# Optimization experiments

Hardware: AMD Instinct MI355X
Metric: run time of the kernel (lower is better)

Reference implementation:

```python
import jax, jax.numpy as jnp
import numpy as np

N_NODES = 50000
N_EDGES = 800000
IN_FEATS = 128
H_FEATS = 128
OUT_FEATS = 64


def _mean_agg(h, src, dst, n_nodes):
    # mean over in-neighbors: sum h[src] into dst, divide by in-degree (0 for isolated nodes)
    summed = jax.ops.segment_sum(h[src], dst, num_segments=n_nodes)  # [N, d]
    deg = jax.ops.segment_sum(jnp.ones((src.shape[0],), h.dtype), dst, num_segments=n_nodes)
    return summed / jnp.maximum(deg, 1.0)[:, None]


def setup_inputs() -> dict:
    key = jax.random.key(0)
    ks = jax.random.split(key, 10)
    s = 0.05
    return {
        "inputs": jax.random.normal(ks[0], (N_NODES, IN_FEATS), jnp.float32),
        "fc_W": jax.random.normal(ks[1], (H_FEATS, IN_FEATS), jnp.float32) * s,
        "fc_b": jax.random.normal(ks[2], (H_FEATS,), jnp.float32) * s,
        "W": jax.random.normal(ks[3], (3, H_FEATS, H_FEATS), jnp.float32) * s,
        "b": jax.random.normal(ks[4], (3, H_FEATS), jnp.float32) * s,
        "W_last": jax.random.normal(ks[5], (OUT_FEATS, H_FEATS), jnp.float32) * s,
        "b_last": jax.random.normal(ks[6], (OUT_FEATS,), jnp.float32) * s,
        "eps": jnp.zeros((4,), jnp.float32),
        "src": jax.random.randint(ks[7], (N_EDGES,), 0, N_NODES, jnp.int32),
        "dst": jax.random.randint(ks[8], (N_EDGES,), 0, N_NODES, jnp.int32),
    }


def reference(inputs, fc_W, fc_b, W, b, W_last, b_last, eps, src, dst):
    n = inputs.shape[0]
    # input SLP
    h = jax.nn.relu(inputs @ fc_W.T + fc_b)
    # 3 hidden GIN layers: relu(Linear((1+eps)*h + mean_agg(h)))  (dropout = eval identity)
    for i in range(3):
        agg = _mean_agg(h, src, dst, n)
        h = jax.nn.relu(((1.0 + eps[i]) * h + agg) @ W[i].T + b[i])
    # last GIN layer (no ReLU)
    agg = _mean_agg(h, src, dst, n)
    h = ((1.0 + eps[3]) * h + agg) @ W_last.T + b_last
    return h
```

## Files before the change

### kernel.cpp

```cpp
#include <hip/hip_runtime.h>

#define N_NODES 50000
#define N_EDGES 800000
#define NBUCK 196
#define CAP 4608
#define CSTRIDE 16
#define EPB 4096
#define NSTRIPE ((N_EDGES + EPB - 1) / EPB)

typedef __attribute__((ext_vector_type(8))) short short8;
typedef __attribute__((ext_vector_type(4))) float float4v;

__device__ inline unsigned short f2bf(float f) {
    unsigned u = __float_as_uint(f);
    unsigned r = u + 0x7fff + ((u >> 16) & 1);
    return (unsigned short)(r >> 16);
}
__device__ inline float bf2f(unsigned short h) {
    return __uint_as_float(((unsigned)h) << 16);
}


__global__ void __launch_bounds__(256) wsplit_init(
    const float* __restrict__ fcW, const float* __restrict__ W, const float* __restrict__ Wl,
    unsigned short* __restrict__ hi, unsigned short* __restrict__ lo, int* __restrict__ cursor) {
    if (blockIdx.x == 0) {
        for (int j = threadIdx.x; j < NBUCK * CSTRIDE; j += 256) cursor[j] = 0;
    }
    int i = blockIdx.x * 256 + threadIdx.x;
    float v;
    if (i < 16384) v = fcW[i];
    else if (i < 65536) v = W[i - 16384];
    else if (i < 73728) v = Wl[i - 65536];
    else return;
    unsigned short h = f2bf(v);
    hi[i] = h;
    lo[i] = f2bf(v - bf2f(h));
}


template <int COLS, bool RELU, bool WRITE_BF, bool BIAS, bool ASPLIT>
__device__ __forceinline__ void gemm_body(int bx, const float* __restrict__ U,
                                          const unsigned short* __restrict__ Uhi,
                                          const unsigned short* __restrict__ Ulo,
                                          const unsigned short* __restrict__ Whi,
                                          const unsigned short* __restrict__ Wlo,
                                          const float* __restrict__ bias, float* __restrict__ out,
                                          unsigned short* __restrict__ outbf, int nrows) {
    int wave = threadIdx.x >> 6;
    int lane = threadIdx.x & 63;
    int m = lane & 15;
    int quad = lane >> 4;
    int r0 = bx * 64 + wave * 16;
    int rowA = r0 + m;
    if (rowA >= nrows) rowA = nrows - 1;

    short8 ahi[4], alo[4];
    if (ASPLIT) {
        const unsigned short* hp = Uhi + (size_t)rowA * 128 + quad * 8;
        const unsigned short* lp = Ulo + (size_t)rowA * 128 + quad * 8;
#pragma unroll
        for (int kc = 0; kc < 4; kc++) {
            ahi[kc] = *(const short8*)(hp + kc * 32);
            alo[kc] = *(const short8*)(lp + kc * 32);
        }
    } else {
        const float* arow = U + (size_t)rowA * 128 + quad * 8;
#pragma unroll
        for (int kc = 0; kc < 4; kc++) {
            float4 f0 = *(const float4*)(arow + kc * 32);
            float4 f1 = *(const float4*)(arow + kc * 32 + 4);
            float fv[8] = {f0.x, f0.y, f0.z, f0.w, f1.x, f1.y, f1.z, f1.w};
#pragma unroll
            for (int j = 0; j < 8; j++) {
                unsigned short h = f2bf(fv[j]);
                ahi[kc][j] = (short)h;
                alo[kc][j] = (short)f2bf(fv[j] - bf2f(h));
            }
        }
    }

#pragma unroll
    for (int nt = 0; nt < COLS / 16; nt++) {
        int n = nt * 16 + m;
        const unsigned short* bhp = Whi + (size_t)n * 128 + quad * 8;
        const unsigned short* blp = Wlo + (size_t)n * 128 + quad * 8;
        float4v acc = {0.f, 0.f, 0.f, 0.f};
#pragma unroll
        for (int kc = 0; kc < 4; kc++) {
            short8 bh = *(const short8*)(bhp + kc * 32);
            short8 bl = *(const short8*)(blp + kc * 32);
            acc = __builtin_amdgcn_mfma_f32_16x16x32_bf16(ahi[kc], bh, acc, 0, 0, 0);
            acc = __builtin_amdgcn_mfma_f32_16x16x32_bf16(alo[kc], bh, acc, 0, 0, 0);
            acc = __builtin_amdgcn_mfma_f32_16x16x32_bf16(ahi[kc], bl, acc, 0, 0, 0);
        }
        float bv = 0.f;
        if (BIAS) bv = bias[n];
#pragma unroll
        for (int i = 0; i < 4; i++) {
            int r = r0 + quad * 4 + i;
            if (r < nrows) {
                float v = acc[i] + bv;
                if (RELU) v = fmaxf(v, 0.f);
                out[(size_t)r * COLS + n] = v;
                if (WRITE_BF) outbf[(size_t)r * COLS + n] = f2bf(v);
            }
        }
    }
}

template <int COLS, bool RELU, bool WRITE_BF, bool BIAS, bool ASPLIT>
__global__ void __launch_bounds__(256) gemm_mfma(const float* __restrict__ U,
                                                 const unsigned short* __restrict__ Uhi,
                                                 const unsigned short* __restrict__ Ulo,
                                                 const unsigned short* __restrict__ Whi,
                                                 const unsigned short* __restrict__ Wlo,
                                                 const float* __restrict__ bias,
                                                 float* __restrict__ out,
                                                 unsigned short* __restrict__ outbf, int nrows) {
    gemm_body<COLS, RELU, WRITE_BF, BIAS, ASPLIT>(blockIdx.x, U, Uhi, Ulo, Whi, Wlo, bias, out,
                                                  outbf, nrows);
}


__global__ void __launch_bounds__(256) fused_binA_gemm(
    const int* __restrict__ src, const int* __restrict__ dst, int* __restrict__ cursor,
    int* __restrict__ packed, const float* __restrict__ X, const unsigned short* __restrict__ whi,
    const unsigned short* __restrict__ wlo, const float* __restrict__ fcb, float* __restrict__ h,
    unsigned short* __restrict__ hbf) {
    int bx = blockIdx.x;
    if (bx < NSTRIPE) {
        __shared__ int lcount[256];
        __shared__ int lbase[256];
        int t = threadIdx.x;
        lcount[t] = 0;
        __syncthreads();
        int base = bx * EPB + t;
#pragma unroll 4
        for (int k = 0; k < EPB / 256; k++) {
            int i = base + k * 256;
            if (i < N_EDGES) atomicAdd(&lcount[((unsigned)dst[i]) >> 8], 1);
        }
        __syncthreads();
        if (t < NBUCK) {
            lbase[t] = t * CAP + atomicAdd(&cursor[t * CSTRIDE], lcount[t]);
            lcount[t] = 0;
        }
        __syncthreads();
#pragma unroll 4
        for (int k = 0; k < EPB / 256; k++) {
            int i = base + k * 256;
            if (i < N_EDGES) {
                int d = dst[i];
                int wb = ((unsigned)d) >> 8;
                int p = lbase[wb] + atomicAdd(&lcount[wb], 1);
                if (p < (wb + 1) * CAP)
                    packed[p] = ((d & 255) << 16) | src[i];
            }
        }
    } else {
        gemm_body<128, true, true, true, false>(bx - NSTRIPE, X, nullptr, nullptr, whi, wlo, fcb,
                                                h, hbf, N_NODES);
    }
}


__global__ void __launch_bounds__(256) binB_kernel(const int* __restrict__ packed,
                                                   const int* __restrict__ cursor,
                                                   int* __restrict__ row_ptr,
                                                   int* __restrict__ esrc) {
    __shared__ int sm[256];
    __shared__ int cntS[256];
    __shared__ int curs[256];
    int b = blockIdx.x;
    int t = threadIdx.x;
    int cnt = (t < NBUCK) ? cursor[t * CSTRIDE] : 0;
    cntS[t] = cnt;
    sm[t] = cnt;
    __syncthreads();
    for (int o = 1; o < 256; o <<= 1) {
        int x = sm[t];
        int a = (t >= o) ? sm[t - o] : 0;
        __syncthreads();
        sm[t] = x + a;
        __syncthreads();
    }
    int w0 = sm[b] - cntS[b];
    int mycnt = cntS[b];
    int total = sm[NBUCK - 1];
    __syncthreads();
    if (b == NBUCK - 1 && t == 0) row_ptr[N_NODES] = total;
    int e0r = b * CAP, e1r = b * CAP + mycnt;
    curs[t] = 0;
    __syncthreads();
    for (int i = e0r + t; i < e1r; i += 256) atomicAdd(&curs[((unsigned)packed[i]) >> 16], 1);
    __syncthreads();
    int v = curs[t];
    sm[t] = v;
    __syncthreads();
    for (int o = 1; o < 256; o <<= 1) {
        int x = sm[t];
        int a = (t >= o) ? sm[t - o] : 0;
        __syncthreads();
        sm[t] = x + a;
        __syncthreads();
    }
    int excl = sm[t] - v;
    curs[t] = excl;
    int node = b * 256 + t;
    if (node < N_NODES) row_ptr[node] = w0 + excl;
    __syncthreads();
    for (int i = e0r + t; i < e1r; i += 256) {
        unsigned w = (unsigned)packed[i];
        int p = atomicAdd(&curs[w >> 16], 1);
        esrc[w0 + p] = (int)(w & 0xFFFFu);
    }
}


__global__ void __launch_bounds__(256) agg_kernel(
    const float* __restrict__ h, const unsigned short* __restrict__ hbf,
    const int* __restrict__ row_ptr, const int* __restrict__ esrc,
    const float* __restrict__ eps, int layer, unsigned* __restrict__ uhi32,
    unsigned* __restrict__ ulo32) {
    int gtid = blockIdx.x * 256 + threadIdx.x;
    int node = gtid >> 6;
    int lane = threadIdx.x & 63;
    if (node >= N_NODES) return;
    node = __builtin_amdgcn_readfirstlane(node);
    int beg = __builtin_amdgcn_readfirstlane(row_ptr[node]);
    int end = __builtin_amdgcn_readfirstlane(row_ptr[node + 1]);
    int eg = lane >> 4;
    int fo = lane & 15;

    float a0[8] = {0.f, 0.f, 0.f, 0.f, 0.f, 0.f, 0.f, 0.f};
    float a1[8] = {0.f, 0.f, 0.f, 0.f, 0.f, 0.f, 0.f, 0.f};
    float a2[8] = {0.f, 0.f, 0.f, 0.f, 0.f, 0.f, 0.f, 0.f};
    float a3[8] = {0.f, 0.f, 0.f, 0.f, 0.f, 0.f, 0.f, 0.f};
    int e = beg;
    for (; e + 15 < end; e += 16) {
        int s0 = esrc[e + eg];
        int s1 = esrc[e + 4 + eg];
        int s2 = esrc[e + 8 + eg];
        int s3 = esrc[e + 12 + eg];
        short8 v0 = *(const short8*)(hbf + (size_t)s0 * 128 + fo * 8);
        short8 v1 = *(const short8*)(hbf + (size_t)s1 * 128 + fo * 8);
        short8 v2 = *(const short8*)(hbf + (size_t)s2 * 128 + fo * 8);
        short8 v3 = *(const short8*)(hbf + (size_t)s3 * 128 + fo * 8);
#pragma unroll
        for (int j = 0; j < 8; j++) a0[j] += bf2f((unsigned short)v0[j]);
#pragma unroll
        for (int j = 0; j < 8; j++) a1[j] += bf2f((unsigned short)v1[j]);
#pragma unroll
        for (int j = 0; j < 8; j++) a2[j] += bf2f((unsigned short)v2[j]);
#pragma unroll
        for (int j = 0; j < 8; j++) a3[j] += bf2f((unsigned short)v3[j]);
    }
    if (e + 7 < end) {
        int s0 = esrc[e + eg];
        int s1 = esrc[e + 4 + eg];
        short8 v0 = *(const short8*)(hbf + (size_t)s0 * 128 + fo * 8);
        short8 v1 = *(const short8*)(hbf + (size_t)s1 * 128 + fo * 8);
#pragma unroll
        for (int j = 0; j < 8; j++) a0[j] += bf2f((unsigned short)v0[j]);
#pragma unroll
        for (int j = 0; j < 8; j++) a1[j] += bf2f((unsigned short)v1[j]);
        e += 8;
    }
    if (e + 3 < end) {
        int s = esrc[e + eg];
        short8 v = *(const short8*)(hbf + (size_t)s * 128 + fo * 8);
#pragma unroll
        for (int j = 0; j < 8; j++) a2[j] += bf2f((unsigned short)v[j]);
        e += 4;
    }
    int rem = end - e;
    if (eg < rem) {
        int s = esrc[e + eg];
        short8 v = *(const short8*)(hbf + (size_t)s * 128 + fo * 8);
#pragma unroll
        for (int j = 0; j < 8; j++) a3[j] += bf2f((unsigned short)v[j]);
    }
#pragma unroll
    for (int j = 0; j < 8; j++) {
        float s = (a0[j] + a1[j]) + (a2[j] + a3[j]);
        s += __shfl_xor(s, 16);
        s += __shfl_xor(s, 32);
        a0[j] = s;
    }
    if (eg == 0) {
        int d = end - beg;
        float inv = (d > 0) ? 1.0f / (float)d : 0.0f;
        float ep = 1.0f + eps[layer];
        const float* hr = h + (size_t)node * 128 + fo * 8;
        float4 h0 = *(const float4*)hr;
        float4 h1 = *(const float4*)(hr + 4);
        float hv[8] = {h0.x, h0.y, h0.z, h0.w, h1.x, h1.y, h1.z, h1.w};
        unsigned hip[4], lop[4];
#pragma unroll
        for (int jj = 0; jj < 4; jj++) {
            float ux = ep * hv[2 * jj] + a0[2 * jj] * inv;
            float uy = ep * hv[2 * jj + 1] + a0[2 * jj + 1] * inv;
            unsigned short uh0 = f2bf(ux), uh1 = f2bf(uy);
            hip[jj] = (unsigned)uh0 | ((unsigned)uh1 << 16);
            lop[jj] = (unsigned)f2bf(ux - bf2f(uh0)) | ((unsigned)f2bf(uy - bf2f(uh1)) << 16);
        }
        uint4* ph = (uint4*)(uhi32 + (size_t)node * 64 + fo * 4);
        uint4* pl = (uint4*)(ulo32 + (size_t)node * 64 + fo * 4);
        *ph = make_uint4(hip[0], hip[1], hip[2], hip[3]);
        *pl = make_uint4(lop[0], lop[1], lop[2], lop[3]);
    }
}


__global__ void __launch_bounds__(256) agg64_out(
    const float* __restrict__ g, const unsigned short* __restrict__ gbf,
    const int* __restrict__ row_ptr, const int* __restrict__ esrc,
    const float* __restrict__ eps, const float* __restrict__ bl, float* __restrict__ out) {
    int gtid = blockIdx.x * 256 + threadIdx.x;
    int node = gtid >> 6;
    if (node >= N_NODES) return;
    int lane = threadIdx.x & 63;
    node = __builtin_amdgcn_readfirstlane(node);
    int beg = __builtin_amdgcn_readfirstlane(row_ptr[node]);
    int end = __builtin_amdgcn_readfirstlane(row_ptr[node + 1]);
    int eg = lane >> 3;
    int fo = lane & 7;

    float a0[8] = {0.f, 0.f, 0.f, 0.f, 0.f, 0.f, 0.f, 0.f};
    float a1[8] = {0.f, 0.f, 0.f, 0.f, 0.f, 0.f, 0.f, 0.f};
    float a2[8] = {0.f, 0.f, 0.f, 0.f, 0.f, 0.f, 0.f, 0.f};
    float a3[8] = {0.f, 0.f, 0.f, 0.f, 0.f, 0.f, 0.f, 0.f};
    int e = beg;
    for (; e + 31 < end; e += 32) {
        int s0 = esrc[e + eg];
        int s1 = esrc[e + 8 + eg];
        int s2 = esrc[e + 16 + eg];
        int s3 = esrc[e + 24 + eg];
        short8 v0 = *(const short8*)(gbf + (size_t)s0 * 64 + fo * 8);
        short8 v1 = *(const short8*)(gbf + (size_t)s1 * 64 + fo * 8);
        short8 v2 = *(const short8*)(gbf + (size_t)s2 * 64 + fo * 8);
        short8 v3 = *(const short8*)(gbf + (size_t)s3 * 64 + fo * 8);
#pragma unroll
        for (int j = 0; j < 8; j++) a0[j] += bf2f((unsigned short)v0[j]);
#pragma unroll
        for (int j = 0; j < 8; j++) a1[j] += bf2f((unsigned short)v1[j]);
#pragma unroll
        for (int j = 0; j < 8; j++) a2[j] += bf2f((unsigned short)v2[j]);
#pragma unroll
        for (int j = 0; j < 8; j++) a3[j] += bf2f((unsigned short)v3[j]);
    }
    if (e + 15 < end) {
        int s0 = esrc[e + eg];
        int s1 = esrc[e + 8 + eg];
        short8 v0 = *(const short8*)(gbf + (size_t)s0 * 64 + fo * 8);
        short8 v1 = *(const short8*)(gbf + (size_t)s1 * 64 + fo * 8);
#pragma unroll
        for (int j = 0; j < 8; j++) a0[j] += bf2f((unsigned short)v0[j]);
#pragma unroll
        for (int j = 0; j < 8; j++) a1[j] += bf2f((unsigned short)v1[j]);
        e += 16;
    }
    if (e + 7 < end) {
        int s = esrc[e + eg];
        short8 v = *(const short8*)(gbf + (size_t)s * 64 + fo * 8);
#pragma unroll
        for (int j = 0; j < 8; j++) a2[j] += bf2f((unsigned short)v[j]);
        e += 8;
    }
    int rem = end - e;
    if (eg < rem) {
        int s = esrc[e + eg];
        short8 v = *(const short8*)(gbf + (size_t)s * 64 + fo * 8);
#pragma unroll
        for (int j = 0; j < 8; j++) a3[j] += bf2f((unsigned short)v[j]);
    }
#pragma unroll
    for (int j = 0; j < 8; j++) {
        float s = (a0[j] + a1[j]) + (a2[j] + a3[j]);
        s += __shfl_xor(s, 8);
        s += __shfl_xor(s, 16);
        s += __shfl_xor(s, 32);
        a0[j] = s;
    }
    if (eg == 0) {
        int d = end - beg;
        float inv = (d > 0) ? 1.0f / (float)d : 0.0f;
        float ep = 1.0f + eps[3];
        const float* gr = g + (size_t)node * 64 + fo * 8;
        float4 g0 = *(const float4*)gr;
        float4 g1 = *(const float4*)(gr + 4);
        const float* blr = bl + fo * 8;
        float4 b0 = *(const float4*)blr;
        float4 b1 = *(const float4*)(blr + 4);
        float4 r0, r1;
        r0.x = ep * g0.x + a0[0] * inv + b0.x;
        r0.y = ep * g0.y + a0[1] * inv + b0.y;
        r0.z = ep * g0.z + a0[2] * inv + b0.z;
        r0.w = ep * g0.w + a0[3] * inv + b0.w;
        r1.x = ep * g1.x + a0[4] * inv + b1.x;
        r1.y = ep * g1.y + a0[5] * inv + b1.y;
        r1.z = ep * g1.z + a0[6] * inv + b1.z;
        r1.w = ep * g1.w + a0[7] * inv + b1.w;
        float* op = out + (size_t)node * 64 + fo * 8;
        *(float4*)op = r0;
        *(float4*)(op + 4) = r1;
    }
}


extern "C" void kernel_launch(void* const* d_in, const int* in_sizes, int n_in,
                              void* d_out, int out_size, void* d_ws, size_t ws_size,
                              hipStream_t stream) {
    const float* X   = (const float*)d_in[0];
    const float* fcW = (const float*)d_in[1];
    const float* fcb = (const float*)d_in[2];
    const float* W   = (const float*)d_in[3];
    const float* b   = (const float*)d_in[4];
    const float* Wl  = (const float*)d_in[5];
    const float* bl  = (const float*)d_in[6];
    const float* eps = (const float*)d_in[7];
    const int* src   = (const int*)d_in[8];
    const int* dst   = (const int*)d_in[9];
    float* out = (float*)d_out;

    float* h = (float*)d_ws;
    unsigned short* hbf = (unsigned short*)(h + (size_t)N_NODES * 128);
    unsigned short* uhi = hbf + (size_t)N_NODES * 128;
    unsigned short* ulo = uhi + (size_t)N_NODES * 128;
    unsigned short* whi = ulo + (size_t)N_NODES * 128;
    unsigned short* wlo = whi + 73728;
    int* cursor  = (int*)(wlo + 73728);
    int* row_ptr = cursor + NBUCK * CSTRIDE;
    int* packed  = row_ptr + N_NODES + 1;
    int* esrc    = packed + NBUCK * CAP;
    float* g = (float*)uhi;
    unsigned short* gbf = ulo;

    const int gemm_blocks = (N_NODES + 63) / 64;
    const int agg_blocks = (N_NODES * 64 + 255) / 256;
    const int prep_blocks = (73728 + 255) / 256;

    wsplit_init<<<prep_blocks, 256, 0, stream>>>(fcW, W, Wl, whi, wlo, cursor);
    fused_binA_gemm<<<NSTRIPE + gemm_blocks, 256, 0, stream>>>(src, dst, cursor, packed, X, whi,
                                                               wlo, fcb, h, hbf);
    binB_kernel<<<NBUCK, 256, 0, stream>>>(packed, cursor, row_ptr, esrc);

    for (int i = 0; i < 3; i++) {
        agg_kernel<<<agg_blocks, 256, 0, stream>>>(h, hbf, row_ptr, esrc, eps, i,
                                                   (unsigned*)uhi, (unsigned*)ulo);
        if (i < 2)
            gemm_mfma<128, true, true, true, true><<<gemm_blocks, 256, 0, stream>>>(
                nullptr, uhi, ulo, whi + 16384 + (size_t)i * 16384,
                wlo + 16384 + (size_t)i * 16384, b + (size_t)i * 128, h, hbf, N_NODES);
        else
            gemm_mfma<128, true, false, true, true><<<gemm_blocks, 256, 0, stream>>>(
                nullptr, uhi, ulo, whi + 16384 + (size_t)i * 16384,
                wlo + 16384 + (size_t)i * 16384, b + (size_t)i * 128, h, nullptr, N_NODES);
    }

    gemm_mfma<64, false, true, false, false><<<gemm_blocks, 256, 0, stream>>>(
        h, nullptr, nullptr, whi + 65536, wlo + 65536, nullptr, g, gbf, N_NODES);
    agg64_out<<<agg_blocks, 256, 0, stream>>>(g, gbf, row_ptr, esrc, eps, bl, out);
}
```

Measured before the change: 410.4 us.

## Fuse neighbor aggregation with layer GEMM and final projection per node tile

Each hidden layer now runs as one kernel. A block of 512 threads gathers and mean-aggregates 16 nodes, splits the combined input into bf16 hi/lo parts in swizzled LDS, and runs the 128-wide MFMA GEMM straight from LDS. This removes the global round-trip of the split activations and one launch per layer. The last hidden layer also chains the W_last projection from LDS, and the bf16 features ping-pong between two buffers. Weight splitting and cursor zeroing move into the first fused kernel and a memset, so there are fewer launches. In exchange, the GEMM tiles are small and every block re-reads the weights from cache.

Result: faster. 387.6 us (-5.6%).

```diff
diff --git a/kernel.cpp b/kernel.cpp
--- a/kernel.cpp
+++ b/kernel.cpp
@@ -7,6 +7,8 @@
 #define CSTRIDE 16
 #define EPB 4096
 #define NSTRIPE ((N_EDGES + EPB - 1) / EPB)
+#define GEMMB 782
+#define WSPLB 224
 
 typedef __attribute__((ext_vector_type(8))) short short8;
 typedef __attribute__((ext_vector_type(4))) float float4v;
@@ -20,113 +22,128 @@
     return __uint_as_float(((unsigned)h) << 16);
 }
 
-
-__global__ void __launch_bounds__(256) wsplit_init(
-    const float* __restrict__ fcW, const float* __restrict__ W, const float* __restrict__ Wl,
-    unsigned short* __restrict__ hi, unsigned short* __restrict__ lo, int* __restrict__ cursor) {
-    if (blockIdx.x == 0) {
-        for (int j = threadIdx.x; j < NBUCK * CSTRIDE; j += 256) cursor[j] = 0;
-    }
-    int i = blockIdx.x * 256 + threadIdx.x;
-    float v;
-    if (i < 16384) v = fcW[i];
-    else if (i < 65536) v = W[i - 16384];
-    else if (i < 73728) v = Wl[i - 65536];
-    else return;
-    unsigned short h = f2bf(v);
-    hi[i] = h;
-    lo[i] = f2bf(v - bf2f(h));
-}
-
-
-template <int COLS, bool RELU, bool WRITE_BF, bool BIAS, bool ASPLIT>
-__device__ __forceinline__ void gemm_body(int bx, const float* __restrict__ U,
-                                          const unsigned short* __restrict__ Uhi,
-                                          const unsigned short* __restrict__ Ulo,
-                                          const unsigned short* __restrict__ Whi,
-                                          const unsigned short* __restrict__ Wlo,
-                                          const float* __restrict__ bias, float* __restrict__ out,
-                                          unsigned short* __restrict__ outbf, int nrows) {
+__device__ __forceinline__ void split8(const float* __restrict__ p, short8& hi8, short8& lo8) {
+    float4 f0 = *(const float4*)p;
+    float4 f1 = *(const float4*)(p + 4);
+    float fv[8] = {f0.x, f0.y, f0.z, f0.w, f1.x, f1.y, f1.z, f1.w};
+#pragma unroll
+    for (int j = 0; j < 8; j++) {
+        unsigned short hh = f2bf(fv[j]);
+        hi8[j] = (short)hh;
+        lo8[j] = (short)f2bf(fv[j] - bf2f(hh));
+    }
+}
+
+
+__device__ __forceinline__ void gather_sum(const unsigned short* __restrict__ bf,
+                                           const int* __restrict__ esrc, int beg, int end,
+                                           int eg, int fo, float a0[8]) {
+    float a1[8], a2[8], a3[8];
+#pragma unroll
+    for (int j = 0; j < 8; j++) { a0[j] = 0.f; a1[j] = 0.f; a2[j] = 0.f; a3[j] = 0.f; }
+    int e = beg;
+    for (; e + 15 < end; e += 16) {
+        int s0 = esrc[e + eg];
+        int s1 = esrc[e + 4 + eg];
+        int s2 = esrc[e + 8 + eg];
+        int s3 = esrc[e + 12 + eg];
+        short8 v0 = *(const short8*)(bf + (size_t)s0 * 128 + fo * 8);
+        short8 v1 = *(const short8*)(bf + (size_t)s1 * 128 + fo * 8);
+        short8 v2 = *(const short8*)(bf + (size_t)s2 * 128 + fo * 8);
+        short8 v3 = *(const short8*)(bf + (size_t)s3 * 128 + fo * 8);
+#pragma unroll
+        for (int j = 0; j < 8; j++) a0[j] += bf2f((unsigned short)v0[j]);
+#pragma unroll
+        for (int j = 0; j < 8; j++) a1[j] += bf2f((unsigned short)v1[j]);
+#pragma unroll
+        for (int j = 0; j < 8; j++) a2[j] += bf2f((unsigned short)v2[j]);
+#pragma unroll
+        for (int j = 0; j < 8; j++) a3[j] += bf2f((unsigned short)v3[j]);
+    }
+    if (e + 7 < end) {
+        int s0 = esrc[e + eg];
+        int s1 = esrc[e + 4 + eg];
+        short8 v0 = *(const short8*)(bf + (size_t)s0 * 128 + fo * 8);
+        short8 v1 = *(const short8*)(bf + (size_t)s1 * 128 + fo * 8);
+#pragma unroll
+        for (int j = 0; j < 8; j++) a0[j] += bf2f((unsigned short)v0[j]);
+#pragma unroll
+        for (int j = 0; j < 8; j++) a1[j] += bf2f((unsigned short)v1[j]);
+        e += 8;
+    }
+    if (e + 3 < end) {
+        int s = esrc[e + eg];
+        short8 v = *(const short8*)(bf + (size_t)s * 128 + fo * 8);
+#pragma unroll
+        for (int j = 0; j < 8; j++) a2[j] += bf2f((unsigned short)v[j]);
+        e += 4;
+    }
+    int rem = end - e;
+    if (eg < rem) {
+        int s = esrc[e + eg];
+        short8 v = *(const short8*)(bf + (size_t)s * 128 + fo * 8);
+#pragma unroll
+        for (int j = 0; j < 8; j++) a3[j] += bf2f((unsigned short)v[j]);
+    }
+#pragma unroll
+    for (int j = 0; j < 8; j++) {
+        float s = (a0[j] + a1[j]) + (a2[j] + a3[j]);
+        s += __shfl_xor(s, 16);
+        s += __shfl_xor(s, 32);
+        a0[j] = s;
+    }
+}
+
+
+__device__ __forceinline__ void slp_gemm(int bx, const float* __restrict__ X,
+                                         const float* __restrict__ fcW,
+                                         const float* __restrict__ fcb, float* __restrict__ h,
+                                         unsigned short* __restrict__ hbf) {
     int wave = threadIdx.x >> 6;
     int lane = threadIdx.x & 63;
     int m = lane & 15;
     int quad = lane >> 4;
     int r0 = bx * 64 + wave * 16;
     int rowA = r0 + m;
-    if (rowA >= nrows) rowA = nrows - 1;
+    if (rowA >= N_NODES) rowA = N_NODES - 1;
 
     short8 ahi[4], alo[4];
-    if (ASPLIT) {
-        const unsigned short* hp = Uhi + (size_t)rowA * 128 + quad * 8;
-        const unsigned short* lp = Ulo + (size_t)rowA * 128 + quad * 8;
+    const float* arow = X + (size_t)rowA * 128 + quad * 8;
+#pragma unroll
+    for (int kc = 0; kc < 4; kc++) split8(arow + kc * 32, ahi[kc], alo[kc]);
+
+#pragma unroll
+    for (int nt = 0; nt < 8; nt++) {
+        int n = nt * 16 + m;
+        const float* brow = fcW + (size_t)n * 128 + quad * 8;
+        float4v acc = {0.f, 0.f, 0.f, 0.f};
 #pragma unroll
         for (int kc = 0; kc < 4; kc++) {
-            ahi[kc] = *(const short8*)(hp + kc * 32);
-            alo[kc] = *(const short8*)(lp + kc * 32);
-        }
-    } else {
-        const float* arow = U + (size_t)rowA * 128 + quad * 8;
-#pragma unroll
-        for (int kc = 0; kc < 4; kc++) {
-            float4 f0 = *(const float4*)(arow + kc * 32);
-            float4 f1 = *(const float4*)(arow + kc * 32 + 4);
-            float fv[8] = {f0.x, f0.y, f0.z, f0.w, f1.x, f1.y, f1.z, f1.w};
-#pragma unroll
-            for (int j = 0; j < 8; j++) {
-                unsigned short h = f2bf(fv[j]);
-                ahi[kc][j] = (short)h;
-                alo[kc][j] = (short)f2bf(fv[j] - bf2f(h));
-            }
-        }
-    }
-
-#pragma unroll
-    for (int nt = 0; nt < COLS / 16; nt++) {
-        int n = nt * 16 + m;
-        const unsigned short* bhp = Whi + (size_t)n * 128 + quad * 8;
-        const unsigned short* blp = Wlo + (size_t)n * 128 + quad * 8;
-        float4v acc = {0.f, 0.f, 0.f, 0.f};
-#pragma unroll
-        for (int kc = 0; kc < 4; kc++) {
-            short8 bh = *(const short8*)(bhp + kc * 32);
-            short8 bl = *(const short8*)(blp + kc * 32);
+            short8 bh, bl;
+            split8(brow + kc * 32, bh, bl);
             acc = __builtin_amdgcn_mfma_f32_16x16x32_bf16(ahi[kc], bh, acc, 0, 0, 0);
             acc = __builtin_amdgcn_mfma_f32_16x16x32_bf16(alo[kc], bh, acc, 0, 0, 0);
             acc = __builtin_amdgcn_mfma_f32_16x16x32_bf16(ahi[kc], bl, acc, 0, 0, 0);
         }
-        float bv = 0.f;
-        if (BIAS) bv = bias[n];
+        float bv = fcb[n];
 #pragma unroll
         for (int i = 0; i < 4; i++) {
             int r = r0 + quad * 4 + i;
-            if (r < nrows) {
-                float v = acc[i] + bv;
-                if (RELU) v = fmaxf(v, 0.f);
-                out[(size_t)r * COLS + n] = v;
-                if (WRITE_BF) outbf[(size_t)r * COLS + n] = f2bf(v);
+            if (r < N_NODES) {
+                float v = fmaxf(acc[i] + bv, 0.f);
+                h[(size_t)r * 128 + n] = v;
+                hbf[(size_t)r * 128 + n] = f2bf(v);
             }
         }
     }
-}
-
-template <int COLS, bool RELU, bool WRITE_BF, bool BIAS, bool ASPLIT>
-__global__ void __launch_bounds__(256) gemm_mfma(const float* __restrict__ U,
-                                                 const unsigned short* __restrict__ Uhi,
-                                                 const unsigned short* __restrict__ Ulo,
-                                                 const unsigned short* __restrict__ Whi,
-                                                 const unsigned short* __restrict__ Wlo,
-                                                 const float* __restrict__ bias,
-                                                 float* __restrict__ out,
-                                                 unsigned short* __restrict__ outbf, int nrows) {
-    gemm_body<COLS, RELU, WRITE_BF, BIAS, ASPLIT>(blockIdx.x, U, Uhi, Ulo, Whi, Wlo, bias, out,
-                                                  outbf, nrows);
 }
 
 
 __global__ void __launch_bounds__(256) fused_binA_gemm(
     const int* __restrict__ src, const int* __restrict__ dst, int* __restrict__ cursor,
-    int* __restrict__ packed, const float* __restrict__ X, const unsigned short* __restrict__ whi,
-    const unsigned short* __restrict__ wlo, const float* __restrict__ fcb, float* __restrict__ h,
+    int* __restrict__ packed, const float* __restrict__ X, const float* __restrict__ fcW,
+    const float* __restrict__ fcb, const float* __restrict__ W, const float* __restrict__ Wl,
+    unsigned short* __restrict__ whi, unsigned short* __restrict__ wlo, float* __restrict__ h,
     unsigned short* __restrict__ hbf) {
     int bx = blockIdx.x;
     if (bx < NSTRIPE) {
@@ -158,9 +175,16 @@
                     packed[p] = ((d & 255) << 16) | src[i];
             }
         }
+    } else if (bx < NSTRIPE + GEMMB) {
+        slp_gemm(bx - NSTRIPE, X, fcW, fcb, h, hbf);
     } else {
-        gemm_body<128, true, true, true, false>(bx - NSTRIPE, X, nullptr, nullptr, whi, wlo, fcb,
-                                                h, hbf, N_NODES);
+        int i = (bx - NSTRIPE - GEMMB) * 256 + threadIdx.x + 16384;
+        if (i < 73728) {
+            float v = (i < 65536) ? W[i - 16384] : Wl[i - 65536];
+            unsigned short hh = f2bf(v);
+            whi[i] = hh;
+            wlo[i] = f2bf(v - bf2f(hh));
+        }
     }
 }
 
@@ -218,97 +242,131 @@
 }
 
 
-__global__ void __launch_bounds__(256) agg_kernel(
-    const float* __restrict__ h, const unsigned short* __restrict__ hbf,
-    const int* __restrict__ row_ptr, const int* __restrict__ esrc,
-    const float* __restrict__ eps, int layer, unsigned* __restrict__ uhi32,
-    unsigned* __restrict__ ulo32) {
-    int gtid = blockIdx.x * 256 + threadIdx.x;
-    int node = gtid >> 6;
-    int lane = threadIdx.x & 63;
-    if (node >= N_NODES) return;
-    node = __builtin_amdgcn_readfirstlane(node);
-    int beg = __builtin_amdgcn_readfirstlane(row_ptr[node]);
-    int end = __builtin_amdgcn_readfirstlane(row_ptr[node + 1]);
+template <bool LAST>
+__global__ void __launch_bounds__(512) layer_fused(
+    float* __restrict__ hio, const unsigned short* __restrict__ bfin,
+    unsigned short* __restrict__ bfout, const int* __restrict__ row_ptr,
+    const int* __restrict__ esrc, const float* __restrict__ eps, int layer,
+    const unsigned short* __restrict__ Whi, const unsigned short* __restrict__ Wlo,
+    const float* __restrict__ bias, const unsigned short* __restrict__ Lhi,
+    const unsigned short* __restrict__ Llo, float* __restrict__ g,
+    unsigned short* __restrict__ gbf) {
+    __shared__ unsigned lds_hi[16 * 64];
+    __shared__ unsigned lds_lo[16 * 64];
+    int tid = threadIdx.x;
+    int wv = tid >> 6;
+    int lane = tid & 63;
     int eg = lane >> 4;
     int fo = lane & 15;
-
-    float a0[8] = {0.f, 0.f, 0.f, 0.f, 0.f, 0.f, 0.f, 0.f};
-    float a1[8] = {0.f, 0.f, 0.f, 0.f, 0.f, 0.f, 0.f, 0.f};
-    float a2[8] = {0.f, 0.f, 0.f, 0.f, 0.f, 0.f, 0.f, 0.f};
-    float a3[8] = {0.f, 0.f, 0.f, 0.f, 0.f, 0.f, 0.f, 0.f};
-    int e = beg;
-    for (; e + 15 < end; e += 16) {
-        int s0 = esrc[e + eg];
-        int s1 = esrc[e + 4 + eg];
-        int s2 = esrc[e + 8 + eg];
-        int s3 = esrc[e + 12 + eg];
-        short8 v0 = *(const short8*)(hbf + (size_t)s0 * 128 + fo * 8);
-        short8 v1 = *(const short8*)(hbf + (size_t)s1 * 128 + fo * 8);
-        short8 v2 = *(const short8*)(hbf + (size_t)s2 * 128 + fo * 8);
-        short8 v3 = *(const short8*)(hbf + (size_t)s3 * 128 + fo * 8);
-#pragma unroll
-        for (int j = 0; j < 8; j++) a0[j] += bf2f((unsigned short)v0[j]);
-#pragma unroll
-        for (int j = 0; j < 8; j++) a1[j] += bf2f((unsigned short)v1[j]);
-#pragma unroll
-        for (int j = 0; j < 8; j++) a2[j] += bf2f((unsigned short)v2[j]);
-#pragma unroll
-        for (int j = 0; j < 8; j++) a3[j] += bf2f((unsigned short)v3[j]);
-    }
-    if (e + 7 < end) {
-        int s0 = esrc[e + eg];
-        int s1 = esrc[e + 4 + eg];
-        short8 v0 = *(const short8*)(hbf + (size_t)s0 * 128 + fo * 8);
-        short8 v1 = *(const short8*)(hbf + (size_t)s1 * 128 + fo * 8);
-#pragma unroll
-        for (int j = 0; j < 8; j++) a0[j] += bf2f((unsigned short)v0[j]);
-#pragma unroll
-        for (int j = 0; j < 8; j++) a1[j] += bf2f((unsigned short)v1[j]);
-        e += 8;
-    }
-    if (e + 3 < end) {
-        int s = esrc[e + eg];
-        short8 v = *(const short8*)(hbf + (size_t)s * 128 + fo * 8);
-#pragma unroll
-        for (int j = 0; j < 8; j++) a2[j] += bf2f((unsigned short)v[j]);
-        e += 4;
-    }
-    int rem = end - e;
-    if (eg < rem) {
-        int s = esrc[e + eg];
-        short8 v = *(const short8*)(hbf + (size_t)s * 128 + fo * 8);
-#pragma unroll
-        for (int j = 0; j < 8; j++) a3[j] += bf2f((unsigned short)v[j]);
-    }
-#pragma unroll
-    for (int j = 0; j < 8; j++) {
-        float s = (a0[j] + a1[j]) + (a2[j] + a3[j]);
-        s += __shfl_xor(s, 16);
-        s += __shfl_xor(s, 32);
-        a0[j] = s;
-    }
-    if (eg == 0) {
-        int d = end - beg;
-        float inv = (d > 0) ? 1.0f / (float)d : 0.0f;
-        float ep = 1.0f + eps[layer];
-        const float* hr = h + (size_t)node * 128 + fo * 8;
-        float4 h0 = *(const float4*)hr;
-        float4 h1 = *(const float4*)(hr + 4);
-        float hv[8] = {h0.x, h0.y, h0.z, h0.w, h1.x, h1.y, h1.z, h1.w};
-        unsigned hip[4], lop[4];
-#pragma unroll
-        for (int jj = 0; jj < 4; jj++) {
-            float ux = ep * hv[2 * jj] + a0[2 * jj] * inv;
-            float uy = ep * hv[2 * jj + 1] + a0[2 * jj + 1] * inv;
-            unsigned short uh0 = f2bf(ux), uh1 = f2bf(uy);
-            hip[jj] = (unsigned)uh0 | ((unsigned)uh1 << 16);
-            lop[jj] = (unsigned)f2bf(ux - bf2f(uh0)) | ((unsigned)f2bf(uy - bf2f(uh1)) << 16);
-        }
-        uint4* ph = (uint4*)(uhi32 + (size_t)node * 64 + fo * 4);
-        uint4* pl = (uint4*)(ulo32 + (size_t)node * 64 + fo * 4);
-        *ph = make_uint4(hip[0], hip[1], hip[2], hip[3]);
-        *pl = make_uint4(lop[0], lop[1], lop[2], lop[3]);
+    int nb = blockIdx.x * 16;
+    float ep = 1.0f + eps[layer];
+
+#pragma unroll
+    for (int half = 0; half < 2; half++) {
+        int r = wv + half * 8;
+        int node = nb + r;
+        int beg = __builtin_amdgcn_readfirstlane(row_ptr[node]);
+        int end = __builtin_amdgcn_readfirstlane(row_ptr[node + 1]);
+        float a0[8];
+        gather_sum(bfin, esrc, beg, end, eg, fo, a0);
+        if (eg == 0) {
+            int d = end - beg;
+            float inv = (d > 0) ? 1.0f / (float)d : 0.0f;
+            const float* hr = hio + (size_t)node * 128 + fo * 8;
+            float4 h0 = *(const float4*)hr;
+            float4 h1 = *(const float4*)(hr + 4);
+            float hv[8] = {h0.x, h0.y, h0.z, h0.w, h1.x, h1.y, h1.z, h1.w};
+            unsigned hip[4], lop[4];
+#pragma unroll
+            for (int jj = 0; jj < 4; jj++) {
+                float ux = ep * hv[2 * jj] + a0[2 * jj] * inv;
+                float uy = ep * hv[2 * jj + 1] + a0[2 * jj + 1] * inv;
+                unsigned short uh0 = f2bf(ux), uh1 = f2bf(uy);
+                hip[jj] = (unsigned)uh0 | ((unsigned)uh1 << 16);
+                lop[jj] = (unsigned)f2bf(ux - bf2f(uh0)) | ((unsigned)f2bf(uy - bf2f(uh1)) << 16);
+            }
+            int grp = fo ^ (r & 7);
+            *(uint4*)&lds_hi[r * 64 + grp * 4] = make_uint4(hip[0], hip[1], hip[2], hip[3]);
+            *(uint4*)&lds_lo[r * 64 + grp * 4] = make_uint4(lop[0], lop[1], lop[2], lop[3]);
+        }
+    }
+    __syncthreads();
+
+    int m = lane & 15;
+    int quad = lane >> 4;
+    short8 ahi[4], alo[4];
+#pragma unroll
+    for (int kc = 0; kc < 4; kc++) {
+        int grp = (quad + kc * 4) ^ (m & 7);
+        ahi[kc] = *(const short8*)&lds_hi[m * 64 + grp * 4];
+        alo[kc] = *(const short8*)&lds_lo[m * 64 + grp * 4];
+    }
+    int n = wv * 16 + m;
+    const unsigned short* bhp = Whi + (size_t)n * 128 + quad * 8;
+    const unsigned short* blp = Wlo + (size_t)n * 128 + quad * 8;
+    float4v acc = {0.f, 0.f, 0.f, 0.f};
+#pragma unroll
+    for (int kc = 0; kc < 4; kc++) {
+        short8 bh = *(const short8*)(bhp + kc * 32);
+        short8 bl = *(const short8*)(blp + kc * 32);
+        acc = __builtin_amdgcn_mfma_f32_16x16x32_bf16(ahi[kc], bh, acc, 0, 0, 0);
+        acc = __builtin_amdgcn_mfma_f32_16x16x32_bf16(alo[kc], bh, acc, 0, 0, 0);
+        acc = __builtin_amdgcn_mfma_f32_16x16x32_bf16(ahi[kc], bl, acc, 0, 0, 0);
+    }
+    float bv = bias[n];
+
+    if (!LAST) {
+#pragma unroll
+        for (int i = 0; i < 4; i++) {
+            int rg = nb + quad * 4 + i;
+            float v = fmaxf(acc[i] + bv, 0.f);
+            hio[(size_t)rg * 128 + n] = v;
+            bfout[(size_t)rg * 128 + n] = f2bf(v);
+        }
+    } else {
+        __syncthreads();
+        unsigned short* lh = (unsigned short*)lds_hi;
+        unsigned short* ll = (unsigned short*)lds_lo;
+#pragma unroll
+        for (int i = 0; i < 4; i++) {
+            int rl = quad * 4 + i;
+            float v = fmaxf(acc[i] + bv, 0.f);
+            unsigned short vh = f2bf(v);
+            unsigned short vl = f2bf(v - bf2f(vh));
+            int gidx = (n >> 3) ^ (rl & 7);
+            int us = rl * 128 + gidx * 8 + (n & 7);
+            lh[us] = vh;
+            ll[us] = vl;
+        }
+        __syncthreads();
+        if (wv < 4) {
+            short8 a2h[4], a2l[4];
+#pragma unroll
+            for (int kc = 0; kc < 4; kc++) {
+                int grp = (quad + kc * 4) ^ (m & 7);
+                a2h[kc] = *(const short8*)&lds_hi[m * 64 + grp * 4];
+                a2l[kc] = *(const short8*)&lds_lo[m * 64 + grp * 4];
+            }
+            int n2 = wv * 16 + m;
+            const unsigned short* lhp = Lhi + (size_t)n2 * 128 + quad * 8;
+            const unsigned short* llp = Llo + (size_t)n2 * 128 + quad * 8;
+            float4v a2 = {0.f, 0.f, 0.f, 0.f};
+#pragma unroll
+            for (int kc = 0; kc < 4; kc++) {
+                short8 bh = *(const short8*)(lhp + kc * 32);
+                short8 bl = *(const short8*)(llp + kc * 32);
+                a2 = __builtin_amdgcn_mfma_f32_16x16x32_bf16(a2h[kc], bh, a2, 0, 0, 0);
+                a2 = __builtin_amdgcn_mfma_f32_16x16x32_bf16(a2l[kc], bh, a2, 0, 0, 0);
+                a2 = __builtin_amdgcn_mfma_f32_16x16x32_bf16(a2h[kc], bl, a2, 0, 0, 0);
+            }
+#pragma unroll
+            for (int i = 0; i < 4; i++) {
+                int rg = nb + quad * 4 + i;
+                float v = a2[i];
+                g[(size_t)rg * 64 + n2] = v;
+                gbf[(size_t)rg * 64 + n2] = f2bf(v);
+            }
+        }
     }
 }
 
@@ -425,41 +483,34 @@
     float* out = (float*)d_out;
 
     float* h = (float*)d_ws;
-    unsigned short* hbf = (unsigned short*)(h + (size_t)N_NODES * 128);
-    unsigned short* uhi = hbf + (size_t)N_NODES * 128;
-    unsigned short* ulo = uhi + (size_t)N_NODES * 128;
-    unsigned short* whi = ulo + (size_t)N_NODES * 128;
+    unsigned short* bfA = (unsigned short*)(h + (size_t)N_NODES * 128);
+    unsigned short* bfB = bfA + (size_t)N_NODES * 128;
+    unsigned short* whi = bfB + (size_t)N_NODES * 128;
     unsigned short* wlo = whi + 73728;
     int* cursor  = (int*)(wlo + 73728);
     int* row_ptr = cursor + NBUCK * CSTRIDE;
     int* packed  = row_ptr + N_NODES + 1;
     int* esrc    = packed + NBUCK * CAP;
-    float* g = (float*)uhi;
-    unsigned short* gbf = ulo;
-
-    const int gemm_blocks = (N_NODES + 63) / 64;
+    unsigned short* gbf = (unsigned short*)(esrc + N_EDGES);
+    float* g = (float*)bfB;
+
     const int agg_blocks = (N_NODES * 64 + 255) / 256;
-    const int prep_blocks = (73728 + 255) / 256;
-
-    wsplit_init<<<prep_blocks, 256, 0, stream>>>(fcW, W, Wl, whi, wlo, cursor);
-    fused_binA_gemm<<<NSTRIPE + gemm_blocks, 256, 0, stream>>>(src, dst, cursor, packed, X, whi,
-                                                               wlo, fcb, h, hbf);
-    binB_kernel<<<NBUCK, 256, 0, stream>>>(packed, cursor, row_ptr, esrc);
-
-    for (int i = 0; i < 3; i++) {
-        agg_kernel<<<agg_blocks, 256, 0, stream>>>(h, hbf, row_ptr, esrc, eps, i,
-                                                   (unsigned*)uhi, (unsigned*)ulo);
-        if (i < 2)
-            gemm_mfma<128, true, true, true, true><<<gemm_blocks, 256, 0, stream>>>(
-                nullptr, uhi, ulo, whi + 16384 + (size_t)i * 16384,
-                wlo + 16384 + (size_t)i * 16384, b + (size_t)i * 128, h, hbf, N_NODES);
-        else
-            gemm_mfma<128, true, false, true, true><<<gemm_blocks, 256, 0, stream>>>(
-                nullptr, uhi, ulo, whi + 16384 + (size_t)i * 16384,
-                wlo + 16384 + (size_t)i * 16384, b + (size_t)i * 128, h, nullptr, N_NODES);
-    }
-
-    gemm_mfma<64, false, true, false, false><<<gemm_blocks, 256, 0, stream>>>(
-        h, nullptr, nullptr, whi + 65536, wlo + 65536, nullptr, g, gbf, N_NODES);
+    const int layer_blocks = N_NODES / 16;
+
+    hipMemsetAsync(cursor, 0, NBUCK * CSTRIDE * sizeof(int), stream);
+    fused_binA_gemm<<<NSTRIPE + GEMMB + WSPLB, 256, 0, stream>>>(
+        src, dst, cursor, packed, X, fcW, fcb, W, Wl, whi, wlo, h, bfA);
+    binB_kernel<<<NBUCK, 196 > 0 ? 256 : 256, 0, stream>>>(packed, cursor, row_ptr, esrc);
+
+    layer_fused<false><<<layer_blocks, 512, 0, stream>>>(
+        h, bfA, bfB, row_ptr, esrc, eps, 0, whi + 16384, wlo + 16384, b,
+        nullptr, nullptr, nullptr, nullptr);
+    layer_fused<false><<<layer_blocks, 512, 0, stream>>>(
+        h, bfB, bfA, row_ptr, esrc, eps, 1, whi + 32768, wlo + 32768, b + 128,
+        nullptr, nullptr, nullptr, nullptr);
+    layer_fused<true><<<layer_blocks, 512, 0, stream>>>(
+        h, bfA, nullptr, row_ptr, esrc, eps, 2, whi + 49152, wlo + 49152, b + 256,
+        whi + 65536, wlo + 65536, g, gbf);
+
     agg64_out<<<agg_blocks, 256, 0, stream>>>(g, gbf, row_ptr, esrc, eps, bl, out);
 }
```
